# Kernel tuning notes

Hardware: AMD Instinct MI355X
Metric: run time of the kernel (lower is better)

The kernel has to match this reference:

```python
import jax, jax.numpy as jnp
import numpy as np

N = 50000      # nodes
E = 800000     # edges (before self loops)
D = 256        # in_features
SMALL = 25     # floor(D/10)


def setup_inputs() -> dict:
    key = jax.random.key(0)
    k1, k2, k3, k4, k5 = jax.random.split(key, 5)
    x = jax.random.normal(k1, (N, D), jnp.float32)
    src = jax.random.randint(k2, (E,), 0, N)
    dst = jax.random.randint(k3, (E,), 0, N)
    Wq = jax.random.normal(k4, (D, SMALL), jnp.float32) / np.float32(np.sqrt(D))
    bq = jnp.zeros((SMALL,), jnp.float32)
    Wk = jax.random.normal(k5, (D, SMALL), jnp.float32) / np.float32(np.sqrt(D))
    bk = jnp.zeros((SMALL,), jnp.float32)
    return {"x": x, "src": src, "dst": dst, "Wq": Wq, "bq": bq, "Wk": Wk, "bk": bk}


def reference(x, src, dst, Wq, bq, Wk, bk):
    d_k = np.float32(np.sqrt(SMALL))  # self.d_k = sqrt(small_in_features)
    q = jnp.tanh(x @ Wq + bq)         # query head: Linear + Tanh, [N, SMALL]
    k = x @ Wk + bk                   # key head: Linear,          [N, SMALL]
    # dgl.add_self_loop: append (i, i) for every node
    loop = jnp.arange(N, dtype=src.dtype)
    s = jnp.concatenate([src, loop])  # [E+N]
    d = jnp.concatenate([dst, loop])  # [E+N]
    # edge weight = <query[src], key[dst]> / d_k
    w = jnp.sum(q[s] * k[d], axis=1) / d_k            # [E+N]
    # segment softmax over incoming edges of each destination node
    wmax = jax.ops.segment_max(w, d, num_segments=N)  # every node has a self loop -> no empty segments
    ew = jnp.exp(w - wmax[d])
    denom = jax.ops.segment_sum(ew, d, num_segments=N)
    alpha = ew / denom[d]                             # [E+N]
    # weighted scatter-sum of src node features
    out = jax.ops.segment_sum(alpha[:, None] * x[s], d, num_segments=N)  # [N, D]
    return out
```

## Files before the change

### kernel.cpp

```cpp
#include <hip/hip_runtime.h>
#include <math.h>

#define D 256
#define SM 25
#define QS 32
#define WROWS 264
#define NCH 4

typedef short bf16x8 __attribute__((ext_vector_type(8)));
typedef float f32x4  __attribute__((ext_vector_type(4)));

__device__ __forceinline__ unsigned int bf16rne(float f) {
    unsigned int u = __float_as_uint(f);
    return (u + 0x7fffu + ((u >> 16) & 1u)) >> 16;
}

__global__ __launch_bounds__(256) void qk_kernel(
    const float* __restrict__ x,
    const float* __restrict__ Wq, const float* __restrict__ bq,
    const float* __restrict__ Wk, const float* __restrict__ bk,
    unsigned short* __restrict__ xh,
    float* __restrict__ qp,
    float* __restrict__ kp,
    int* __restrict__ cnt, int N) {
    __shared__ __align__(16) short xs[64 * WROWS];
    __shared__ __align__(16) short wt[64 * WROWS];
    __shared__ float bias[64];
    int t = threadIdx.x;
    int n0 = blockIdx.x * 64;

    int gid = blockIdx.x * 256 + t;
    if (gid < N) cnt[gid] = 0;

    {
        int r = t >> 2, qtr = t & 3;
        int row = n0 + r; if (row >= N) row = N - 1;
        const float4* xr = (const float4*)(x + (size_t)row * D) + qtr * 16;
        short* dst = xs + r * WROWS + qtr * 64;
#pragma unroll
        for (int i = 0; i < 16; ++i) {
            float4 a = xr[i];
            unsigned int w0 = bf16rne(a.x) | (bf16rne(a.y) << 16);
            unsigned int w1 = bf16rne(a.z) | (bf16rne(a.w) << 16);
            *(uint2*)(dst + i * 4) = make_uint2(w0, w1);
        }
    }
    for (int idx = t; idx < 64 * D; idx += 256) {
        int j = idx >> 8, k = idx & 255;
        float w = 0.f;
        if (j < SM) w = Wq[k * SM + j];
        else if (j < 2 * SM) w = Wk[k * SM + (j - SM)];
        wt[j * WROWS + k] = (short)bf16rne(w);
    }
    if (t < 64) bias[t] = (t < SM) ? bq[t] : ((t < 2 * SM) ? bk[t - SM] : 0.f);
    __syncthreads();

    for (int o = 0; o < 8; ++o) {
        int idx = o * 256 + t;
        int r = idx >> 5, c = idx & 31;
        int row = n0 + r;
        if (row < N) {
            uint4 v = *(const uint4*)(xs + r * WROWS + c * 8);
            *((uint4*)(xh + (size_t)row * D) + c) = v;
        }
    }

    int wid = t >> 6, lane = t & 63;
    int mm = lane & 15, g = lane >> 4;
    f32x4 acc[4];
#pragma unroll
    for (int tt = 0; tt < 4; ++tt) acc[tt] = (f32x4){0.f, 0.f, 0.f, 0.f};
    const short* arow = xs + (wid * 16 + mm) * WROWS + g * 8;
#pragma unroll
    for (int ks = 0; ks < 8; ++ks) {
        bf16x8 af = *(const bf16x8*)(arow + ks * 32);
#pragma unroll
        for (int tt = 0; tt < 4; ++tt) {
            bf16x8 bf = *(const bf16x8*)(wt + (tt * 16 + mm) * WROWS + g * 8 + ks * 32);
            acc[tt] = __builtin_amdgcn_mfma_f32_16x16x32_bf16(af, bf, acc[tt], 0, 0, 0);
        }
    }
#pragma unroll
    for (int tt = 0; tt < 4; ++tt) {
        int j = tt * 16 + mm;
#pragma unroll
        for (int r = 0; r < 4; ++r) {
            int node = n0 + wid * 16 + g * 4 + r;
            if (node >= N) continue;
            float v = acc[tt][r] + bias[j];
            if (j < SM)           qp[(size_t)node * QS + j] = tanhf(v);
            else if (j < 2 * SM)  kp[(size_t)node * QS + (j - SM)] = v;
            else if (j < 57)      qp[(size_t)node * QS + (j - SM)] = 0.f;
            else                  kp[(size_t)node * QS + (j - 32)] = 0.f;
        }
    }
}

__global__ void hist_kernel(const int4* __restrict__ dst4, int* __restrict__ cnt, int n4e) {
    int e = blockIdx.x * blockDim.x + threadIdx.x;
    if (e >= n4e) return;
    int4 d = dst4[e];
    atomicAdd(&cnt[d.x], 1);
    atomicAdd(&cnt[d.y], 1);
    atomicAdd(&cnt[d.z], 1);
    atomicAdd(&cnt[d.w], 1);
}

__global__ __launch_bounds__(256) void scan_a_kernel(const int4* __restrict__ cnt4,
                                                     int* __restrict__ bsum, int n4) {
    __shared__ int wsum[4];
    int t = threadIdx.x;
    int idx = blockIdx.x * 256 + t;
    int s = 0;
    if (idx < n4) { int4 v = cnt4[idx]; s = v.x + v.y + v.z + v.w; }
#pragma unroll
    for (int o = 32; o; o >>= 1) s += __shfl_xor(s, o);
    if ((t & 63) == 0) wsum[t >> 6] = s;
    __syncthreads();
    if (t == 0) bsum[blockIdx.x] = wsum[0] + wsum[1] + wsum[2] + wsum[3];
}

__global__ __launch_bounds__(64) void scan_b_kernel(const int* __restrict__ bsum,
                                                    int* __restrict__ bbase,
                                                    int* __restrict__ offN, int nblk) {
    int lane = threadIdx.x;
    int v = (lane < nblk) ? bsum[lane] : 0;
    int incl = v;
#pragma unroll
    for (int o = 1; o < 64; o <<= 1) {
        int u = __shfl_up(incl, o);
        if (lane >= o) incl += u;
    }
    bbase[lane] = incl - v;
    if (lane == 63) *offN = incl;
}

__global__ __launch_bounds__(256) void scan_c_kernel(const int4* __restrict__ cnt4,
                                                     const int* __restrict__ bbase,
                                                     int4* __restrict__ off4,
                                                     int4* __restrict__ cursor4, int n4) {
    __shared__ int wsum[4];
    int t = threadIdx.x;
    int idx = blockIdx.x * 256 + t;
    int4 v = make_int4(0, 0, 0, 0);
    if (idx < n4) v = cnt4[idx];
    int s0 = v.x, s01 = s0 + v.y, s012 = s01 + v.z, s = s012 + v.w;
    int lane = t & 63;
    int incl = s;
#pragma unroll
    for (int o = 1; o < 64; o <<= 1) {
        int u = __shfl_up(incl, o);
        if (lane >= o) incl += u;
    }
    if (lane == 63) wsum[t >> 6] = incl;
    __syncthreads();
    int w = t >> 6;
    int wbase = 0;
    for (int i = 0; i < w; ++i) wbase += wsum[i];
    int base = bbase[blockIdx.x] + wbase + (incl - s);
    if (idx < n4) {
        int4 o4 = make_int4(base, base + s0, base + s01, base + s012);
        off4[idx]    = o4;
        cursor4[idx] = o4;
    }
}

__global__ void scatter_kernel(const int4* __restrict__ src4, const int4* __restrict__ dst4,
                               int* __restrict__ cursor, int* __restrict__ csr_src, int n4e) {
    int e = blockIdx.x * blockDim.x + threadIdx.x;
    if (e >= n4e) return;
    int4 s = src4[e];
    int4 d = dst4[e];
    csr_src[atomicAdd(&cursor[d.x], 1)] = s.x;
    csr_src[atomicAdd(&cursor[d.y], 1)] = s.y;
    csr_src[atomicAdd(&cursor[d.z], 1)] = s.z;
    csr_src[atomicAdd(&cursor[d.w], 1)] = s.w;
}

__global__ __launch_bounds__(256) void agg_kernel(
        const uint2* __restrict__ xh2, const float* __restrict__ qp,
        const float* __restrict__ kp, const int* __restrict__ off,
        const int* __restrict__ csr_src, float4* __restrict__ out4, int N) {
    int lane = threadIdx.x & 63;
    int v = blockIdx.x * 4 + (threadIdx.x >> 6);
    if (v >= N) return;
    int lo = off[v];
    int deg1 = off[v + 1] - lo + 1;
    const float4* kd4 = (const float4*)(kp + (size_t)v * QS);
    float4 kd[6];
#pragma unroll
    for (int j = 0; j < 6; ++j) kd[j] = kd4[j];
    float kd24 = kp[(size_t)v * QS + 24];

    float wv[NCH]; int sv[NCH];
    float m = -INFINITY;
#pragma unroll
    for (int c = 0; c < NCH; ++c) {
        int i = c * 64 + lane;
        float wcur = -INFINITY; int s = v;
        if (c * 64 < deg1 && i < deg1) {
            if (i > 0) s = csr_src[lo + i - 1];
            const float4* q4 = (const float4*)(qp + (size_t)s * QS);
            float acc = qp[(size_t)s * QS + 24] * kd24;
#pragma unroll
            for (int j = 0; j < 6; ++j) {
                float4 a = q4[j];
                acc += a.x*kd[j].x + a.y*kd[j].y + a.z*kd[j].z + a.w*kd[j].w;
            }
            wcur = acc * 0.2f;
        }
        wv[c] = wcur; sv[c] = s;
        m = fmaxf(m, wcur);
    }
#pragma unroll
    for (int o = 32; o; o >>= 1) m = fmaxf(m, __shfl_xor(m, o));
    float ssum = 0.f;
#pragma unroll
    for (int c = 0; c < NCH; ++c) {
        float e = (wv[c] == -INFINITY) ? 0.f : __expf(wv[c] - m);
        wv[c] = e;
        ssum += e;
    }
#pragma unroll
    for (int o = 32; o; o >>= 1) ssum += __shfl_xor(ssum, o);
    float inv = 1.f / ssum;

    float4 acc = make_float4(0.f, 0.f, 0.f, 0.f);
#pragma unroll
    for (int c = 0; c < NCH; ++c) {
        if (c * 64 >= deg1) break;
        int cnt = deg1 - c * 64; if (cnt > 64) cnt = 64;
        for (int j = 0; j < cnt; ++j) {
            float a = __shfl(wv[c], j);
            int   s = __shfl(sv[c], j);
            uint2 hx = xh2[(size_t)s * 64 + lane];
            float f0 = __uint_as_float(hx.x << 16);
            float f1 = __uint_as_float(hx.x & 0xffff0000u);
            float f2 = __uint_as_float(hx.y << 16);
            float f3 = __uint_as_float(hx.y & 0xffff0000u);
            acc.x += a * f0; acc.y += a * f1; acc.z += a * f2; acc.w += a * f3;
        }
    }
    acc.x *= inv; acc.y *= inv; acc.z *= inv; acc.w *= inv;
    out4[(size_t)v * 64 + lane] = acc;
}

extern "C" void kernel_launch(void* const* d_in, const int* in_sizes, int n_in,
                              void* d_out, int out_size, void* d_ws, size_t ws_size,
                              hipStream_t stream) {
    const float* x   = (const float*)d_in[0];
    const int*   src = (const int*)d_in[1];
    const int*   dst = (const int*)d_in[2];
    const float* Wq  = (const float*)d_in[3];
    const float* bq  = (const float*)d_in[4];
    const float* Wk  = (const float*)d_in[5];
    const float* bk  = (const float*)d_in[6];
    float* out = (float*)d_out;

    int N = in_sizes[0] / D;
    int E = in_sizes[1];

    char* p = (char*)d_ws;
    auto alloc = [&](size_t bytes) {
        char* r = p;
        p += (bytes + 255) & ~(size_t)255;
        return r;
    };
    unsigned short* xh = (unsigned short*)alloc((size_t)N * D * sizeof(unsigned short));
    float* qp      = (float*)alloc((size_t)N * QS * sizeof(float));
    float* kp      = (float*)alloc((size_t)N * QS * sizeof(float));
    int*   cnt     = (int*)  alloc((size_t)(N + 4) * sizeof(int));
    int*   off     = (int*)  alloc((size_t)(N + 4) * sizeof(int));
    int*   cursor  = (int*)  alloc((size_t)(N + 4) * sizeof(int));
    int*   csr_src = (int*)  alloc((size_t)E * sizeof(int));
    int*   bsum    = (int*)  alloc(64 * sizeof(int));
    int*   bbase   = (int*)  alloc(64 * sizeof(int));

    int nqk = (N + 63) / 64;
    qk_kernel<<<nqk, 256, 0, stream>>>(x, Wq, bq, Wk, bk, xh, qp, kp, cnt, N);
    int n4e = E / 4;
    hist_kernel<<<(n4e + 255) / 256, 256, 0, stream>>>((const int4*)dst, cnt, n4e);
    int n4 = (N + 3) / 4;
    int nblk = (n4 + 255) / 256;
    scan_a_kernel<<<nblk, 256, 0, stream>>>((const int4*)cnt, bsum, n4);
    scan_b_kernel<<<1, 64, 0, stream>>>(bsum, bbase, off + N, nblk);
    scan_c_kernel<<<nblk, 256, 0, stream>>>((const int4*)cnt, bbase,
                                            (int4*)off, (int4*)cursor, n4);
    scatter_kernel<<<(n4e + 255) / 256, 256, 0, stream>>>(
        (const int4*)src, (const int4*)dst, cursor, csr_src, n4e);
    agg_kernel<<<(N + 3) / 4, 256, 0, stream>>>(
        (const uint2*)xh, qp, kp, off, csr_src, (float4*)out, N);
}
```

Measured before the change: 316.5 us.

## Fuse histogram into qk, merge scan passes, precompute weights, unroll gather

Weight conversion to bf16 and bias packing move into a small prep kernel that also zeroes counts. The per-block weight conversion in qk becomes a vectorized copy. The degree histogram is folded into the tail of qk_kernel, and the block-sum scan is merged into scan_c, removing two launches. The aggregation gather loop is unrolled by 4 so multiple row loads are in flight at once. Tail handling for E not divisible by 4 is added, at the cost of a serial loop in one thread.

```diff
diff --git a/kernel.cpp b/kernel.cpp
--- a/kernel.cpp
+++ b/kernel.cpp
@@ -14,24 +14,48 @@
     unsigned int u = __float_as_uint(f);
     return (u + 0x7fffu + ((u >> 16) & 1u)) >> 16;
 }
+__device__ __forceinline__ float bl(unsigned int lo16) {
+    return __uint_as_float(lo16 << 16);
+}
+__device__ __forceinline__ float bh(unsigned int u) {
+    return __uint_as_float(u & 0xffff0000u);
+}
+
+__global__ __launch_bounds__(256) void prep_kernel(
+    const float* __restrict__ Wq, const float* __restrict__ bq,
+    const float* __restrict__ Wk, const float* __restrict__ bk,
+    unsigned short* __restrict__ wt_g,
+    float* __restrict__ bias_g,
+    int* __restrict__ cnt, int N) {
+    int gid = blockIdx.x * 256 + threadIdx.x;
+    if (gid < N) cnt[gid] = 0;
+    if (gid < 64 * 256) {
+        int j = gid >> 8, k = gid & 255;
+        float w = 0.f;
+        if (j < SM) w = Wq[k * SM + j];
+        else if (j < 2 * SM) w = Wk[k * SM + (j - SM)];
+        wt_g[j * 256 + k] = (unsigned short)bf16rne(w);
+    }
+    if (gid >= 16384 && gid < 16448) {
+        int t = gid - 16384;
+        bias_g[t] = (t < SM) ? bq[t] : ((t < 2 * SM) ? bk[t - SM] : 0.f);
+    }
+}
 
 __global__ __launch_bounds__(256) void qk_kernel(
     const float* __restrict__ x,
-    const float* __restrict__ Wq, const float* __restrict__ bq,
-    const float* __restrict__ Wk, const float* __restrict__ bk,
+    const unsigned short* __restrict__ wt_g, const float* __restrict__ bias_g,
+    const int4* __restrict__ dst4, const int* __restrict__ dste,
     unsigned short* __restrict__ xh,
     float* __restrict__ qp,
     float* __restrict__ kp,
-    int* __restrict__ cnt, int N) {
+    int* __restrict__ cnt, int N, int E) {
     __shared__ __align__(16) short xs[64 * WROWS];
     __shared__ __align__(16) short wt[64 * WROWS];
     __shared__ float bias[64];
     int t = threadIdx.x;
     int n0 = blockIdx.x * 64;
 
-    int gid = blockIdx.x * 256 + t;
-    if (gid < N) cnt[gid] = 0;
-
     {
         int r = t >> 2, qtr = t & 3;
         int row = n0 + r; if (row >= N) row = N - 1;
@@ -45,14 +69,13 @@
             *(uint2*)(dst + i * 4) = make_uint2(w0, w1);
         }
     }
-    for (int idx = t; idx < 64 * D; idx += 256) {
-        int j = idx >> 8, k = idx & 255;
-        float w = 0.f;
-        if (j < SM) w = Wq[k * SM + j];
-        else if (j < 2 * SM) w = Wk[k * SM + (j - SM)];
-        wt[j * WROWS + k] = (short)bf16rne(w);
-    }
-    if (t < 64) bias[t] = (t < SM) ? bq[t] : ((t < 2 * SM) ? bk[t - SM] : 0.f);
+#pragma unroll
+    for (int o = 0; o < 8; ++o) {
+        int idx = o * 256 + t;
+        int j = idx >> 5, k8 = idx & 31;
+        *(uint4*)(wt + j * WROWS + k8 * 8) = ((const uint4*)wt_g)[idx];
+    }
+    if (t < 64) bias[t] = bias_g[t];
     __syncthreads();
 
     for (int o = 0; o < 8; ++o) {
@@ -94,16 +117,19 @@
             else                  kp[(size_t)node * QS + (j - 32)] = 0.f;
         }
     }
-}
-
-__global__ void hist_kernel(const int4* __restrict__ dst4, int* __restrict__ cnt, int n4e) {
-    int e = blockIdx.x * blockDim.x + threadIdx.x;
-    if (e >= n4e) return;
-    int4 d = dst4[e];
-    atomicAdd(&cnt[d.x], 1);
-    atomicAdd(&cnt[d.y], 1);
-    atomicAdd(&cnt[d.z], 1);
-    atomicAdd(&cnt[d.w], 1);
+
+    int gid = blockIdx.x * 256 + t;
+    int n4e = E >> 2;
+    if (gid < n4e) {
+        int4 dd = dst4[gid];
+        atomicAdd(&cnt[dd.x], 1);
+        atomicAdd(&cnt[dd.y], 1);
+        atomicAdd(&cnt[dd.z], 1);
+        atomicAdd(&cnt[dd.w], 1);
+    }
+    if (gid == 0) {
+        for (int e = n4e * 4; e < E; ++e) atomicAdd(&cnt[dste[e]], 1);
+    }
 }
 
 __global__ __launch_bounds__(256) void scan_a_kernel(const int4* __restrict__ cnt4,
@@ -120,32 +146,29 @@
     if (t == 0) bsum[blockIdx.x] = wsum[0] + wsum[1] + wsum[2] + wsum[3];
 }
 
-__global__ __launch_bounds__(64) void scan_b_kernel(const int* __restrict__ bsum,
-                                                    int* __restrict__ bbase,
-                                                    int* __restrict__ offN, int nblk) {
-    int lane = threadIdx.x;
-    int v = (lane < nblk) ? bsum[lane] : 0;
-    int incl = v;
-#pragma unroll
-    for (int o = 1; o < 64; o <<= 1) {
-        int u = __shfl_up(incl, o);
-        if (lane >= o) incl += u;
-    }
-    bbase[lane] = incl - v;
-    if (lane == 63) *offN = incl;
-}
-
 __global__ __launch_bounds__(256) void scan_c_kernel(const int4* __restrict__ cnt4,
-                                                     const int* __restrict__ bbase,
+                                                     const int* __restrict__ bsum,
+                                                     int* __restrict__ offN,
                                                      int4* __restrict__ off4,
-                                                     int4* __restrict__ cursor4, int n4) {
+                                                     int4* __restrict__ cursor4,
+                                                     int n4, int nblk) {
     __shared__ int wsum[4];
     int t = threadIdx.x;
+    int lane = t & 63;
+    int bv = (lane < nblk) ? bsum[lane] : 0;
+    int bincl = bv;
+#pragma unroll
+    for (int o = 1; o < 64; o <<= 1) {
+        int u = __shfl_up(bincl, o);
+        if (lane >= o) bincl += u;
+    }
+    int blockbase = __shfl(bincl - bv, blockIdx.x);
+    int total = __shfl(bincl, nblk - 1);
+    if (blockIdx.x == 0 && t == 0) *offN = total;
     int idx = blockIdx.x * 256 + t;
     int4 v = make_int4(0, 0, 0, 0);
     if (idx < n4) v = cnt4[idx];
     int s0 = v.x, s01 = s0 + v.y, s012 = s01 + v.z, s = s012 + v.w;
-    int lane = t & 63;
     int incl = s;
 #pragma unroll
     for (int o = 1; o < 64; o <<= 1) {
@@ -157,7 +180,7 @@
     int w = t >> 6;
     int wbase = 0;
     for (int i = 0; i < w; ++i) wbase += wsum[i];
-    int base = bbase[blockIdx.x] + wbase + (incl - s);
+    int base = blockbase + wbase + (incl - s);
     if (idx < n4) {
         int4 o4 = make_int4(base, base + s0, base + s01, base + s012);
         off4[idx]    = o4;
@@ -166,7 +189,9 @@
 }
 
 __global__ void scatter_kernel(const int4* __restrict__ src4, const int4* __restrict__ dst4,
-                               int* __restrict__ cursor, int* __restrict__ csr_src, int n4e) {
+                               const int* __restrict__ srce, const int* __restrict__ dste,
+                               int* __restrict__ cursor, int* __restrict__ csr_src,
+                               int n4e, int E) {
     int e = blockIdx.x * blockDim.x + threadIdx.x;
     if (e >= n4e) return;
     int4 s = src4[e];
@@ -175,6 +200,10 @@
     csr_src[atomicAdd(&cursor[d.y], 1)] = s.y;
     csr_src[atomicAdd(&cursor[d.z], 1)] = s.z;
     csr_src[atomicAdd(&cursor[d.w], 1)] = s.w;
+    if (e == 0) {
+        for (int i = n4e * 4; i < E; ++i)
+            csr_src[atomicAdd(&cursor[dste[i]], 1)] = srce[i];
+    }
 }
 
 __global__ __launch_bounds__(256) void agg_kernel(
@@ -230,15 +259,31 @@
     for (int c = 0; c < NCH; ++c) {
         if (c * 64 >= deg1) break;
         int cnt = deg1 - c * 64; if (cnt > 64) cnt = 64;
-        for (int j = 0; j < cnt; ++j) {
+        int j = 0;
+        for (; j + 4 <= cnt; j += 4) {
+            float a0 = __shfl(wv[c], j);     int s0 = __shfl(sv[c], j);
+            float a1 = __shfl(wv[c], j + 1); int s1 = __shfl(sv[c], j + 1);
+            float a2 = __shfl(wv[c], j + 2); int s2 = __shfl(sv[c], j + 2);
+            float a3 = __shfl(wv[c], j + 3); int s3 = __shfl(sv[c], j + 3);
+            uint2 u0 = xh2[(size_t)s0 * 64 + lane];
+            uint2 u1 = xh2[(size_t)s1 * 64 + lane];
+            uint2 u2 = xh2[(size_t)s2 * 64 + lane];
+            uint2 u3 = xh2[(size_t)s3 * 64 + lane];
+            acc.x += a0 * bl(u0.x); acc.y += a0 * bh(u0.x);
+            acc.z += a0 * bl(u0.y); acc.w += a0 * bh(u0.y);
+            acc.x += a1 * bl(u1.x); acc.y += a1 * bh(u1.x);
+            acc.z += a1 * bl(u1.y); acc.w += a1 * bh(u1.y);
+            acc.x += a2 * bl(u2.x); acc.y += a2 * bh(u2.x);
+            acc.z += a2 * bl(u2.y); acc.w += a2 * bh(u2.y);
+            acc.x += a3 * bl(u3.x); acc.y += a3 * bh(u3.x);
+            acc.z += a3 * bl(u3.y); acc.w += a3 * bh(u3.y);
+        }
+        for (; j < cnt; ++j) {
             float a = __shfl(wv[c], j);
             int   s = __shfl(sv[c], j);
-            uint2 hx = xh2[(size_t)s * 64 + lane];
-            float f0 = __uint_as_float(hx.x << 16);
-            float f1 = __uint_as_float(hx.x & 0xffff0000u);
-            float f2 = __uint_as_float(hx.y << 16);
-            float f3 = __uint_as_float(hx.y & 0xffff0000u);
-            acc.x += a * f0; acc.y += a * f1; acc.z += a * f2; acc.w += a * f3;
+            uint2 u = xh2[(size_t)s * 64 + lane];
+            acc.x += a * bl(u.x); acc.y += a * bh(u.x);
+            acc.z += a * bl(u.y); acc.w += a * bh(u.y);
         }
     }
     acc.x *= inv; acc.y *= inv; acc.z *= inv; acc.w *= inv;
@@ -266,7 +311,9 @@
         p += (bytes + 255) & ~(size_t)255;
         return r;
     };
-    unsigned short* xh = (unsigned short*)alloc((size_t)N * D * sizeof(unsigned short));
+    unsigned short* xh   = (unsigned short*)alloc((size_t)N * D * sizeof(unsigned short));
+    unsigned short* wt_g = (unsigned short*)alloc(64 * 256 * sizeof(unsigned short));
+    float* bias_g  = (float*)alloc(64 * sizeof(float));
     float* qp      = (float*)alloc((size_t)N * QS * sizeof(float));
     float* kp      = (float*)alloc((size_t)N * QS * sizeof(float));
     int*   cnt     = (int*)  alloc((size_t)(N + 4) * sizeof(int));
@@ -274,20 +321,21 @@
     int*   cursor  = (int*)  alloc((size_t)(N + 4) * sizeof(int));
     int*   csr_src = (int*)  alloc((size_t)E * sizeof(int));
     int*   bsum    = (int*)  alloc(64 * sizeof(int));
-    int*   bbase   = (int*)  alloc(64 * sizeof(int));
-
+
+    int prepgrid = (N > 16448 ? N : 16448);
+    prep_kernel<<<(prepgrid + 255) / 256, 256, 0, stream>>>(
+        Wq, bq, Wk, bk, wt_g, bias_g, cnt, N);
     int nqk = (N + 63) / 64;
-    qk_kernel<<<nqk, 256, 0, stream>>>(x, Wq, bq, Wk, bk, xh, qp, kp, cnt, N);
-    int n4e = E / 4;
-    hist_kernel<<<(n4e + 255) / 256, 256, 0, stream>>>((const int4*)dst, cnt, n4e);
+    qk_kernel<<<nqk, 256, 0, stream>>>(x, wt_g, bias_g, (const int4*)dst, dst,
+                                       xh, qp, kp, cnt, N, E);
     int n4 = (N + 3) / 4;
     int nblk = (n4 + 255) / 256;
     scan_a_kernel<<<nblk, 256, 0, stream>>>((const int4*)cnt, bsum, n4);
-    scan_b_kernel<<<1, 64, 0, stream>>>(bsum, bbase, off + N, nblk);
-    scan_c_kernel<<<nblk, 256, 0, stream>>>((const int4*)cnt, bbase,
-                                            (int4*)off, (int4*)cursor, n4);
+    scan_c_kernel<<<nblk, 256, 0, stream>>>((const int4*)cnt, bsum, off + N,
+                                            (int4*)off, (int4*)cursor, n4, nblk);
+    int n4e = E / 4;
     scatter_kernel<<<(n4e + 255) / 256, 256, 0, stream>>>(
-        (const int4*)src, (const int4*)dst, cursor, csr_src, n4e);
+        (const int4*)src, (const int4*)dst, src, dst, cursor, csr_src, n4e, E);
     agg_kernel<<<(N + 3) / 4, 256, 0, stream>>>(
         (const uint2*)xh, qp, kp, off, csr_src, (float4*)out, N);
 }
```

Result: faster. 278.4 us (-12.0%).
